# Kernel optimization log

Measured on AMD Instinct MI355X. Metric: run time of the kernel, lower is better.

The kernel has to match this reference:

```python
import jax, jax.numpy as jnp
import numpy as np

EMBED_DIM = 64
CODEBOOK_SIZE = 1024


def setup_inputs() -> dict:
    key = jax.random.key(0)
    k1, k2 = jax.random.split(key)
    inputs = jax.random.normal(k1, (32, 4096, EMBED_DIM), dtype=jnp.float32)
    # codebook stored as (embedding_dim, codebook_size), as in the TF layer
    embeddings = jax.random.normal(k2, (EMBED_DIM, CODEBOOK_SIZE), dtype=jnp.float32)
    return {"inputs": inputs, "embeddings": embeddings}


def reference(inputs, embeddings):
    # inputs: [B, T, D]; embeddings: [D, K]
    B, T, D = inputs.shape
    K = embeddings.shape[1]
    flat = inputs.reshape(-1, D)  # [N, D]
    similarity = flat @ embeddings  # [N, K]
    distances = (
        jnp.sum(flat * flat, axis=1, keepdims=True)
        - 2.0 * similarity
        + jnp.sum(embeddings * embeddings, axis=0, keepdims=True)
    )
    # temperature==0 / inference path -> plain argmax(-distances) == argmin(distances)
    encoding_indices_flat = jnp.argmin(distances, axis=1)  # [N]
    encodings = jax.nn.one_hot(encoding_indices_flat, K, dtype=jnp.float32)  # [N, K]
    encoding_indices = encoding_indices_flat.reshape(B, T)
    # embedding lookup on transposed codebook: [K, D] gathered -> [B, T, D]
    quantized = embeddings.T[encoding_indices]
    # straight-through estimator
    quantized_st = inputs + jax.lax.stop_gradient(quantized - inputs)
    return quantized_st, encodings, encoding_indices
```

## Files before the change

kernel.cpp:

```cpp
#include <hip/hip_runtime.h>

#define D 64
#define K 1024
#define NTOK (32 * 4096)
#define Q_ELEMS ((size_t)NTOK * D)
#define OH_ELEMS ((size_t)NTOK * K)

typedef short bf16x8 __attribute__((ext_vector_type(8)));
typedef float f32x4 __attribute__((ext_vector_type(4)));

#define WS_ETF_OFF 4096
#define WS_ETH_OFF (4096 + 262144)
#define WS_ETL_OFF (4096 + 262144 + 131072)
#define WS_NEED    (4096 + 262144 + 131072 + 131072)

__device__ __forceinline__ unsigned short f2bf(float f) {
    unsigned u = __float_as_uint(f);
    unsigned r = u + 0x7FFFu + ((u >> 16) & 1u);
    return (unsigned short)(r >> 16);
}
__device__ __forceinline__ float bf2f(unsigned short h) {
    return __uint_as_float(((unsigned)h) << 16);
}

__global__ void prep_kernel(const float* __restrict__ E, float* __restrict__ ws) {
    int k = blockIdx.x * 256 + threadIdx.x;
    float* e2 = ws;
    float* etf = (float*)((char*)ws + WS_ETF_OFF);
    unsigned short* ethF = (unsigned short*)((char*)ws + WS_ETH_OFF);
    unsigned short* etlF = (unsigned short*)((char*)ws + WS_ETL_OFF);

    const int tile = k >> 6, ct = (k >> 4) & 3, l15 = k & 15;
    float s = 0.f;
    #pragma unroll
    for (int d = 0; d < D; ++d) {
        float v = E[d * K + k];
        s = fmaf(v, v, s);
        etf[k * D + d] = v;
        unsigned short h = f2bf(v);
        unsigned short l = f2bf(v - bf2f(h));
        const int ks = d >> 5, g = (d >> 3) & 3, j = d & 7;
        const int slot = (((tile * 4 + ct) * 2 + ks) * 64 + g * 16 + l15) * 8 + j;
        ethF[slot] = h;
        etlF[slot] = l;
    }
    e2[k] = s;
}

__device__ __attribute__((noinline)) int rescore_token(
    const float* __restrict__ X, const float* __restrict__ E,
    const float* __restrict__ e2g, int tok, int lane)
{
    const float* xr = X + (size_t)tok * D;
    float bestv = 3.4e38f; int besti = 0;
    #pragma unroll 1
    for (int sb = 0; sb < 2; ++sb) {
        const int k0 = lane * 16 + sb * 8;
        float dot[8] = {0.f,0.f,0.f,0.f,0.f,0.f,0.f,0.f};
        #pragma unroll 1
        for (int db = 0; db < 4; ++db) {
            float4 xc0 = *reinterpret_cast<const float4*>(xr + db * 16 + 0);
            float4 xc1 = *reinterpret_cast<const float4*>(xr + db * 16 + 4);
            float4 xc2 = *reinterpret_cast<const float4*>(xr + db * 16 + 8);
            float4 xc3 = *reinterpret_cast<const float4*>(xr + db * 16 + 12);
            float xs[16] = {xc0.x,xc0.y,xc0.z,xc0.w, xc1.x,xc1.y,xc1.z,xc1.w,
                            xc2.x,xc2.y,xc2.z,xc2.w, xc3.x,xc3.y,xc3.z,xc3.w};
            #pragma unroll
            for (int dd = 0; dd < 16; ++dd) {
                const int d = db * 16 + dd;
                float4 e0 = *reinterpret_cast<const float4*>(E + (size_t)d * K + k0);
                float4 e1 = *reinterpret_cast<const float4*>(E + (size_t)d * K + k0 + 4);
                dot[0] = fmaf(xs[dd], e0.x, dot[0]); dot[1] = fmaf(xs[dd], e0.y, dot[1]);
                dot[2] = fmaf(xs[dd], e0.z, dot[2]); dot[3] = fmaf(xs[dd], e0.w, dot[3]);
                dot[4] = fmaf(xs[dd], e1.x, dot[4]); dot[5] = fmaf(xs[dd], e1.y, dot[5]);
                dot[6] = fmaf(xs[dd], e1.z, dot[6]); dot[7] = fmaf(xs[dd], e1.w, dot[7]);
            }
        }
        float4 ez0 = *reinterpret_cast<const float4*>(e2g + k0);
        float4 ez1 = *reinterpret_cast<const float4*>(e2g + k0 + 4);
        float ezs[8] = {ez0.x,ez0.y,ez0.z,ez0.w, ez1.x,ez1.y,ez1.z,ez1.w};
        #pragma unroll
        for (int j = 0; j < 8; ++j) {
            float dist = fmaf(-2.f, dot[j], ezs[j]);
            if (dist < bestv) { bestv = dist; besti = k0 + j; }
        }
    }
    #pragma unroll
    for (int mm = 1; mm <= 32; mm <<= 1) {
        float ob = __shfl_xor(bestv, mm, 64);
        int   oi = __shfl_xor(besti, mm, 64);
        bool take = (ob < bestv) || (ob == bestv && oi < besti);
        bestv = take ? ob : bestv;
        besti = take ? oi : besti;
    }
    return besti;
}

__global__ __launch_bounds__(256, 2) void vq_mfma_kernel(
    const float* __restrict__ X,
    const float* __restrict__ E,
    const float* __restrict__ ws_f,
    float* __restrict__ qout,
    float* __restrict__ oneh,
    float* __restrict__ idxout)
{
    __shared__ __align__(16) unsigned short btile[2][2][8][512];

    const int lane   = threadIdx.x & 63;
    const int wv     = threadIdx.x >> 6;
    const int lane15 = lane & 15;
    const int g      = lane >> 4;
    const int tokbase = blockIdx.x * 128 + wv * 32;

    const float* e2g = ws_f;
    const float* etf = (const float*)((const char*)ws_f + WS_ETF_OFF);
    const char* ethB = (const char*)ws_f + WS_ETH_OFF;
    const char* etlB = (const char*)ws_f + WS_ETL_OFF;

    bf16x8 ah[2][2], al[2][2];
    #pragma unroll
    for (int mt = 0; mt < 2; ++mt) {
        const float* xr = X + (size_t)(tokbase + mt * 16 + lane15) * D + g * 8;
        #pragma unroll
        for (int ks = 0; ks < 2; ++ks) {
            float4 v0 = *reinterpret_cast<const float4*>(xr + ks * 32);
            float4 v1 = *reinterpret_cast<const float4*>(xr + ks * 32 + 4);
            float xv[8] = {v0.x,v0.y,v0.z,v0.w, v1.x,v1.y,v1.z,v1.w};
            #pragma unroll
            for (int j = 0; j < 8; ++j) {
                unsigned short h = f2bf(xv[j]);
                ah[mt][ks][j] = (short)h;
                al[mt][ks][j] = (short)f2bf(xv[j] - bf2f(h));
            }
        }
    }

    float bb[2][4] = {{3.4e38f,3.4e38f,3.4e38f,3.4e38f},{3.4e38f,3.4e38f,3.4e38f,3.4e38f}};
    float b2[2][4] = {{3.4e38f,3.4e38f,3.4e38f,3.4e38f},{3.4e38f,3.4e38f,3.4e38f,3.4e38f}};
    int   bi[2][4] = {{0,0,0,0},{0,0,0,0}};

    float4 stg0, stg1, stg2, stg3;
    #define LOAD_TILE(T)                                                              \
        do {                                                                          \
            const int c0 = wv * 4;                                                    \
            const char* s0 = ((c0+0) < 8 ? ethB : etlB) + (size_t)(T)*8192 + ((c0+0)&7)*1024; \
            const char* s1 = ((c0+1) < 8 ? ethB : etlB) + (size_t)(T)*8192 + ((c0+1)&7)*1024; \
            const char* s2 = ((c0+2) < 8 ? ethB : etlB) + (size_t)(T)*8192 + ((c0+2)&7)*1024; \
            const char* s3 = ((c0+3) < 8 ? ethB : etlB) + (size_t)(T)*8192 + ((c0+3)&7)*1024; \
            stg0 = reinterpret_cast<const float4*>(s0)[lane];                         \
            stg1 = reinterpret_cast<const float4*>(s1)[lane];                         \
            stg2 = reinterpret_cast<const float4*>(s2)[lane];                         \
            stg3 = reinterpret_cast<const float4*>(s3)[lane];                         \
        } while (0)
    #define WRITE_TILE(B)                                                             \
        do {                                                                          \
            const int c0 = wv * 4;                                                    \
            reinterpret_cast<float4*>(&btile[B][(c0+0)>>3][(c0+0)&7][0])[lane] = stg0; \
            reinterpret_cast<float4*>(&btile[B][(c0+1)>>3][(c0+1)&7][0])[lane] = stg1; \
            reinterpret_cast<float4*>(&btile[B][(c0+2)>>3][(c0+2)&7][0])[lane] = stg2; \
            reinterpret_cast<float4*>(&btile[B][(c0+3)>>3][(c0+3)&7][0])[lane] = stg3; \
        } while (0)

    LOAD_TILE(0);
    WRITE_TILE(0);

    #pragma unroll 1
    for (int tile = 0; tile < 16; ++tile) {
        const int buf = tile & 1;
        __syncthreads();
        if (tile < 15) LOAD_TILE(tile + 1);

        #pragma unroll
        for (int ct = 0; ct < 4; ++ct) {
            const int code = tile * 64 + ct * 16 + lane15;
            f32x4 acc0 = {0.f,0.f,0.f,0.f};
            f32x4 acc1 = {0.f,0.f,0.f,0.f};
            #pragma unroll
            for (int ks = 0; ks < 2; ++ks) {
                const int slot = ct * 2 + ks;
                bf16x8 bh = reinterpret_cast<const bf16x8*>(&btile[buf][0][slot][0])[lane];
                bf16x8 bl = reinterpret_cast<const bf16x8*>(&btile[buf][1][slot][0])[lane];
                acc0 = __builtin_amdgcn_mfma_f32_16x16x32_bf16(ah[0][ks], bh, acc0, 0, 0, 0);
                acc0 = __builtin_amdgcn_mfma_f32_16x16x32_bf16(ah[0][ks], bl, acc0, 0, 0, 0);
                acc0 = __builtin_amdgcn_mfma_f32_16x16x32_bf16(al[0][ks], bh, acc0, 0, 0, 0);
                acc1 = __builtin_amdgcn_mfma_f32_16x16x32_bf16(ah[1][ks], bh, acc1, 0, 0, 0);
                acc1 = __builtin_amdgcn_mfma_f32_16x16x32_bf16(ah[1][ks], bl, acc1, 0, 0, 0);
                acc1 = __builtin_amdgcn_mfma_f32_16x16x32_bf16(al[1][ks], bh, acc1, 0, 0, 0);
            }
            const float e2v = e2g[code];
            #pragma unroll
            for (int r = 0; r < 4; ++r) {
                float d0 = fmaf(-2.f, acc0[r], e2v);
                b2[0][r] = fminf(b2[0][r], fmaxf(bb[0][r], d0));
                if (d0 < bb[0][r]) { bb[0][r] = d0; bi[0][r] = code; }
                float d1 = fmaf(-2.f, acc1[r], e2v);
                b2[1][r] = fminf(b2[1][r], fmaxf(bb[1][r], d1));
                if (d1 < bb[1][r]) { bb[1][r] = d1; bi[1][r] = code; }
            }
        }

        if (tile < 15) WRITE_TILE((tile + 1) & 1);
    }

    #pragma unroll
    for (int m = 1; m <= 8; m <<= 1) {
        #pragma unroll
        for (int mt = 0; mt < 2; ++mt) {
            #pragma unroll
            for (int r = 0; r < 4; ++r) {
                float ob = __shfl_xor(bb[mt][r], m, 64);
                float o2 = __shfl_xor(b2[mt][r], m, 64);
                int   oi = __shfl_xor(bi[mt][r], m, 64);
                float nb2 = fminf(fminf(b2[mt][r], o2), fmaxf(bb[mt][r], ob));
                bool take = (ob < bb[mt][r]) || (ob == bb[mt][r] && oi < bi[mt][r]);
                bb[mt][r] = take ? ob : bb[mt][r];
                bi[mt][r] = take ? oi : bi[mt][r];
                b2[mt][r] = nb2;
            }
        }
    }

    #pragma unroll
    for (int mt = 0; mt < 2; ++mt) {
        #pragma unroll
        for (int r = 0; r < 4; ++r) {
            bool flag = (b2[mt][r] - bb[mt][r]) < 0.125f;
            unsigned long long m = __ballot(flag);
            if (m) {
                #pragma unroll
                for (int gg = 0; gg < 4; ++gg) {
                    if ((m >> (gg * 16)) & 1ULL) {
                        int ei = rescore_token(X, E, e2g, tokbase + mt * 16 + gg * 4 + r, lane);
                        if (g == gg) bi[mt][r] = ei;
                    }
                }
            }
        }
    }

    #pragma unroll
    for (int t = 0; t < 32; ++t) {
        const int t16 = t & 15;
        const int fi = __shfl(bi[t >> 4][t16 & 3], (t16 >> 2) * 16, 64);
        const size_t tok = (size_t)tokbase + t;

        float q  = etf[(size_t)fi * D + lane];
        float xv = X[tok * D + lane];
        __builtin_nontemporal_store(xv + (q - xv), qout + tok * D + lane);

        if (lane == t) idxout[tok] = (float)fi;

        f32x4* row = reinterpret_cast<f32x4*>(oneh + tok * (size_t)K);
        #pragma unroll
        for (int c = 0; c < 4; ++c) {
            const int c4 = (c * 64 + lane) * 4;
            f32x4 v;
            v[0] = (fi == c4 + 0) ? 1.f : 0.f;
            v[1] = (fi == c4 + 1) ? 1.f : 0.f;
            v[2] = (fi == c4 + 2) ? 1.f : 0.f;
            v[3] = (fi == c4 + 3) ? 1.f : 0.f;
            __builtin_nontemporal_store(v, row + c * 64 + lane);
        }
    }
}

__global__ __launch_bounds__(256, 2) void vq_fallback_kernel(
    const float* __restrict__ X, const float* __restrict__ E,
    float* __restrict__ qout, float* __restrict__ oneh, float* __restrict__ idxout)
{
    __shared__ float e2s[K];
    __shared__ int   idxs[256];
    const int tid = threadIdx.x;
    const int tok = blockIdx.x * 256 + tid;
    for (int k = tid; k < K; k += 256) {
        float s = 0.f;
        #pragma unroll
        for (int d = 0; d < D; ++d) { float v = E[d * K + k]; s = fmaf(v, v, s); }
        e2s[k] = s;
    }
    __syncthreads();
    float x[D];
    {
        const float* xp = X + (size_t)tok * D;
        #pragma unroll
        for (int j = 0; j < D / 4; ++j) {
            float4 v = *reinterpret_cast<const float4*>(xp + 4 * j);
            x[4*j+0]=v.x; x[4*j+1]=v.y; x[4*j+2]=v.z; x[4*j+3]=v.w;
        }
    }
    float best = 3.4e38f; int bidx = 0;
    for (int t0 = 0; t0 < K; t0 += 16) {
        float acc[16];
        #pragma unroll
        for (int j = 0; j < 16; ++j) acc[j] = 0.f;
        #pragma unroll
        for (int d = 0; d < D; ++d) {
            const float* ep = E + d * K + t0;
            #pragma unroll
            for (int j = 0; j < 16; ++j) acc[j] = fmaf(x[d], ep[j], acc[j]);
        }
        #pragma unroll
        for (int j = 0; j < 16; ++j) {
            float dist = fmaf(-2.f, acc[j], e2s[t0 + j]);
            if (dist < best) { best = dist; bidx = t0 + j; }
        }
    }
    idxs[tid] = bidx;
    {
        float q[D];
        const float* ec = E + bidx;
        #pragma unroll
        for (int d = 0; d < D; ++d) q[d] = ec[d * K];
        float* qp = qout + (size_t)tok * D;
        #pragma unroll
        for (int j = 0; j < D / 4; ++j) {
            float4 v;
            v.x = x[4*j+0] + (q[4*j+0] - x[4*j+0]);
            v.y = x[4*j+1] + (q[4*j+1] - x[4*j+1]);
            v.z = x[4*j+2] + (q[4*j+2] - x[4*j+2]);
            v.w = x[4*j+3] + (q[4*j+3] - x[4*j+3]);
            *reinterpret_cast<float4*>(qp + 4 * j) = v;
        }
    }
    idxout[tok] = (float)bidx;
    __syncthreads();
    {
        float4* base = reinterpret_cast<float4*>(oneh + (size_t)blockIdx.x * 256 * K);
        for (int i = tid; i < 256 * K / 4; i += 256) {
            int row = i >> 8, c4 = (i & 255) * 4, id = idxs[row];
            float4 v;
            v.x = (id == c4 + 0) ? 1.f : 0.f;
            v.y = (id == c4 + 1) ? 1.f : 0.f;
            v.z = (id == c4 + 2) ? 1.f : 0.f;
            v.w = (id == c4 + 3) ? 1.f : 0.f;
            base[i] = v;
        }
    }
}

extern "C" void kernel_launch(void* const* d_in, const int* in_sizes, int n_in,
                              void* d_out, int out_size, void* d_ws, size_t ws_size,
                              hipStream_t stream) {
    const float* X = (const float*)d_in[0];
    const float* E = (const float*)d_in[1];
    float* qout   = (float*)d_out;
    float* oneh   = qout + Q_ELEMS;
    float* idxout = oneh + OH_ELEMS;

    if (ws_size >= (size_t)WS_NEED) {
        float* ws = (float*)d_ws;
        prep_kernel<<<K / 256, 256, 0, stream>>>(E, ws);
        vq_mfma_kernel<<<NTOK / 128, 256, 0, stream>>>(X, E, ws, qout, oneh, idxout);
    } else {
        vq_fallback_kernel<<<NTOK / 256, 256, 0, stream>>>(X, E, qout, oneh, idxout);
    }
}
```

Before: 214.9 us.

## Interleave one-hot zero stores with distance MFMA loop and rotate codebook tile order

The kernel now streams zeros for each wave's one-hot rows from inside the codebook tile loop, so the large one-hot write traffic overlaps with the MFMA distance computation. After argmin, it scatters a single 1.0 per token and writes the index, following a full waitcnt. Each block also starts its codebook sweep at a different tile (blockIdx mod 16) to spread concurrent reads of the workspace. The rotation changes the order in which codes are scanned, which could alter tie-breaking if the argmin update does not compare indices. Ordering the late 1.0 store after the earlier nontemporal zero stores relies on the waitcnt.

```diff
diff --git a/kernel.cpp b/kernel.cpp
--- a/kernel.cpp
+++ b/kernel.cpp
@@ -111,6 +111,7 @@
     const int lane15 = lane & 15;
     const int g      = lane >> 4;
     const int tokbase = blockIdx.x * 128 + wv * 32;
+    const int bstart  = blockIdx.x & 15;
 
     const float* e2g = ws_f;
     const float* etf = (const float*)((const char*)ws_f + WS_ETF_OFF);
@@ -139,14 +140,18 @@
     float b2[2][4] = {{3.4e38f,3.4e38f,3.4e38f,3.4e38f},{3.4e38f,3.4e38f,3.4e38f,3.4e38f}};
     int   bi[2][4] = {{0,0,0,0},{0,0,0,0}};
 
+    f32x4* ohz = reinterpret_cast<f32x4*>(oneh + (size_t)tokbase * K);
+    const f32x4 zv = {0.f, 0.f, 0.f, 0.f};
+
     float4 stg0, stg1, stg2, stg3;
     #define LOAD_TILE(T)                                                              \
         do {                                                                          \
+            const int rt = ((T) + bstart) & 15;                                       \
             const int c0 = wv * 4;                                                    \
-            const char* s0 = ((c0+0) < 8 ? ethB : etlB) + (size_t)(T)*8192 + ((c0+0)&7)*1024; \
-            const char* s1 = ((c0+1) < 8 ? ethB : etlB) + (size_t)(T)*8192 + ((c0+1)&7)*1024; \
-            const char* s2 = ((c0+2) < 8 ? ethB : etlB) + (size_t)(T)*8192 + ((c0+2)&7)*1024; \
-            const char* s3 = ((c0+3) < 8 ? ethB : etlB) + (size_t)(T)*8192 + ((c0+3)&7)*1024; \
+            const char* s0 = ((c0+0) < 8 ? ethB : etlB) + (size_t)rt*8192 + ((c0+0)&7)*1024; \
+            const char* s1 = ((c0+1) < 8 ? ethB : etlB) + (size_t)rt*8192 + ((c0+1)&7)*1024; \
+            const char* s2 = ((c0+2) < 8 ? ethB : etlB) + (size_t)rt*8192 + ((c0+2)&7)*1024; \
+            const char* s3 = ((c0+3) < 8 ? ethB : etlB) + (size_t)rt*8192 + ((c0+3)&7)*1024; \
             stg0 = reinterpret_cast<const float4*>(s0)[lane];                         \
             stg1 = reinterpret_cast<const float4*>(s1)[lane];                         \
             stg2 = reinterpret_cast<const float4*>(s2)[lane];                         \
@@ -171,8 +176,13 @@
         if (tile < 15) LOAD_TILE(tile + 1);
 
         #pragma unroll
+        for (int zi = 0; zi < 8; ++zi)
+            __builtin_nontemporal_store(zv, ohz + (tile * 8 + zi) * 64 + lane);
+
+        const int rtile = (tile + bstart) & 15;
+        #pragma unroll
         for (int ct = 0; ct < 4; ++ct) {
-            const int code = tile * 64 + ct * 16 + lane15;
+            const int code = rtile * 64 + ct * 16 + lane15;
             f32x4 acc0 = {0.f,0.f,0.f,0.f};
             f32x4 acc1 = {0.f,0.f,0.f,0.f};
             #pragma unroll
@@ -238,29 +248,23 @@
         }
     }
 
+    int fi_lane = 0;
     #pragma unroll
     for (int t = 0; t < 32; ++t) {
         const int t16 = t & 15;
         const int fi = __shfl(bi[t >> 4][t16 & 3], (t16 >> 2) * 16, 64);
+        if ((lane & 31) == t) fi_lane = fi;
+
         const size_t tok = (size_t)tokbase + t;
-
         float q  = etf[(size_t)fi * D + lane];
         float xv = X[tok * D + lane];
         __builtin_nontemporal_store(xv + (q - xv), qout + tok * D + lane);
-
-        if (lane == t) idxout[tok] = (float)fi;
-
-        f32x4* row = reinterpret_cast<f32x4*>(oneh + tok * (size_t)K);
-        #pragma unroll
-        for (int c = 0; c < 4; ++c) {
-            const int c4 = (c * 64 + lane) * 4;
-            f32x4 v;
-            v[0] = (fi == c4 + 0) ? 1.f : 0.f;
-            v[1] = (fi == c4 + 1) ? 1.f : 0.f;
-            v[2] = (fi == c4 + 2) ? 1.f : 0.f;
-            v[3] = (fi == c4 + 3) ? 1.f : 0.f;
-            __builtin_nontemporal_store(v, row + c * 64 + lane);
-        }
+    }
+
+    __builtin_amdgcn_s_waitcnt(0);
+    if (lane < 32) {
+        oneh[(size_t)(tokbase + lane) * K + fi_lane] = 1.0f;
+        idxout[tokbase + lane] = (float)fi_lane;
     }
 }
 
```

New measurement: 227.8 us. +6.0%, slower.
